# Kernel tuning notes

Hardware: AMD Instinct MI355X
Metric: run time of the kernel (lower is better)

Reference implementation:

```python
import jax, jax.numpy as jnp
import numpy as np

B, S, H = 2, 2048, 1024
NH, NKV, HD = 16, 16, 64
R, KF = 16, 4
THETA = 1000000.0


def setup_inputs() -> dict:
    key = jax.random.key(0)
    ks = jax.random.split(key, 16)
    sc = 0.02
    signs = jax.random.randint(ks[13], (1, 1, 1, KF, HD // 2), 0, 2).astype(jnp.float32) * 2 - 1
    cdma = jnp.concatenate([signs, signs], axis=-1)  # [1,1,1,KF,HD]
    return {
        "hidden_states": jax.random.normal(ks[0], (B, S, H), jnp.float32),
        "position_ids": jnp.broadcast_to(jnp.arange(S, dtype=jnp.int32), (B, S)),
        "q_w": jax.random.normal(ks[1], (H, H), jnp.float32) * sc,
        "q_b": jax.random.normal(ks[2], (H,), jnp.float32) * sc,
        "k_w": jax.random.normal(ks[3], (H, H), jnp.float32) * sc,
        "k_b": jax.random.normal(ks[4], (H,), jnp.float32) * sc,
        "v_w": jax.random.normal(ks[5], (H, H), jnp.float32) * sc,
        "v_b": jax.random.normal(ks[6], (H,), jnp.float32) * sc,
        "o_w": jax.random.normal(ks[7], (H, H), jnp.float32) * sc,
        "lora_qA": jax.random.normal(ks[8], (R, H), jnp.float32) * sc,
        "lora_qB": jax.random.normal(ks[9], (H, R), jnp.float32) * sc,
        "lora_vA": jax.random.normal(ks[10], (R, H), jnp.float32) * sc,
        "lora_vB": jax.random.normal(ks[11], (H, R), jnp.float32) * sc,
        "cdma_keys": cdma,
    }


def _rope(q, k, position_ids):
    # cos/sin per HF rotary embedding, theta=1e6 (Qwen1.5)
    inv_freq = 1.0 / (THETA ** (jnp.arange(0, HD, 2, dtype=jnp.float32) / HD))  # [HD/2]
    freqs = position_ids.astype(jnp.float32)[..., None] * inv_freq  # [B,S,HD/2]
    emb = jnp.concatenate([freqs, freqs], axis=-1)  # [B,S,HD]
    cos = jnp.cos(emb)[:, None]  # [B,1,S,HD]
    sin = jnp.sin(emb)[:, None]

    def rot_half(x):
        return jnp.concatenate([-x[..., HD // 2:], x[..., :HD // 2]], axis=-1)

    return q * cos + rot_half(q) * sin, k * cos + rot_half(k) * sin


def reference(hidden_states, position_ids, q_w, q_b, k_w, k_b, v_w, v_b, o_w,
              lora_qA, lora_qB, lora_vA, lora_vB, cdma_keys):
    bsz, q_len, _ = hidden_states.shape
    # base projections + LoRA adjustments (k has no LoRA)
    q = hidden_states @ q_w.T + q_b + (hidden_states @ lora_qA.T) @ lora_qB.T
    k = hidden_states @ k_w.T + k_b
    v = hidden_states @ v_w.T + v_b + (hidden_states @ lora_vA.T) @ lora_vB.T

    q = q.reshape(bsz, q_len, NH, HD).transpose(0, 2, 1, 3)   # [B,NH,S,HD]
    k = k.reshape(bsz, q_len, NKV, HD).transpose(0, 2, 1, 3)  # [B,NKV,S,HD]
    v = v.reshape(bsz, q_len, NKV, HD).transpose(0, 2, 1, 3)

    q, k = _rope(q, k, position_ids)

    # holographic block sign-bind/sum transform (q_len divisible by KF -> no pad)
    n_slots = q_len // KF
    k_blocks = k.reshape(bsz, NKV, n_slots, KF, HD)
    v_blocks = v.reshape(bsz, NKV, n_slots, KF, HD)
    S_K = jnp.sum(k_blocks * cdma_keys, axis=3, keepdims=True)  # [B,NKV,slots,1,HD]
    S_V = jnp.sum(v_blocks * cdma_keys, axis=3, keepdims=True)
    K_noisy = (S_K * cdma_keys).reshape(bsz, NKV, q_len, HD)
    V_noisy = (S_V * cdma_keys).reshape(bsz, NKV, q_len, HD)

    scale = 1.0 / (np.sqrt(HD) * np.sqrt(KF))
    scores = jnp.einsum('bhqd,bhkd->bhqk', q, K_noisy) * scale
    causal = jnp.tril(jnp.ones((q_len, q_len), dtype=bool))
    scores = jnp.where(causal, scores, jnp.float32(-1e9))
    attn = jax.nn.softmax(scores, axis=-1)
    out = jnp.einsum('bhqk,bhkd->bhqd', attn, V_noisy)
    out = out.transpose(0, 2, 1, 3).reshape(bsz, q_len, NH * HD)
    return out @ o_w.T
```

## Files before the change

kernel.cpp:

```cpp
#include <hip/hip_runtime.h>
#include <hip/hip_bf16.h>
#include <math.h>


typedef __bf16 bf16;
typedef __attribute__((ext_vector_type(8))) __bf16 bf16x8;
typedef __attribute__((ext_vector_type(4))) float f32x4;

#define NB 2
#define SEQ 2048
#define HID 1024
#define NHD 16
#define HDD 64

__device__ __forceinline__ void gld_lds16(const void* g, void* l) {
  __builtin_amdgcn_global_load_lds(
      (const __attribute__((address_space(1))) void*)g,
      (__attribute__((address_space(3))) void*)l, 16, 0, 0);
}

__device__ __forceinline__ unsigned pack2bf(float a, float b) {
  unsigned short ua = __builtin_bit_cast(unsigned short, (bf16)a);
  unsigned short ub = __builtin_bit_cast(unsigned short, (bf16)b);
  return ((unsigned)ub << 16) | ua;
}

__global__ __launch_bounds__(256) void prep_wqkv(
    const float* __restrict__ qw, const float* __restrict__ kw,
    const float* __restrict__ vw, const float* __restrict__ qA,
    const float* __restrict__ qB, const float* __restrict__ vA,
    const float* __restrict__ vB, bf16* __restrict__ W) {
  int idx = blockIdx.x * 256 + threadIdx.x;
  if (idx >= 3072 * 1024) return;
  int n = idx >> 10, k = idx & 1023;
  float v;
  if (n < 1024) {
    v = qw[n * 1024 + k];
#pragma unroll
    for (int r = 0; r < 16; ++r) v += qB[n * 16 + r] * qA[r * 1024 + k];
  } else if (n < 2048) {
    v = kw[(n - 1024) * 1024 + k];
  } else {
    int nn = n - 2048;
    v = vw[nn * 1024 + k];
#pragma unroll
    for (int r = 0; r < 16; ++r) v += vB[nn * 16 + r] * vA[r * 1024 + k];
  }
  int seg = k >> 6, cl = k & 63;
  int ch = (cl >> 3) ^ (n & 7);
  W[(size_t)n * 1024 + (seg << 6) + (ch << 3) + (cl & 7)] = (bf16)v;
}

__global__ __launch_bounds__(256) void cvt_swz(const float* __restrict__ src,
                                               bf16* __restrict__ dst,
                                               int total, int cols) {
  int idx = blockIdx.x * 256 + threadIdx.x;
  if (idx >= total) return;
  int r = idx / cols, c = idx - r * cols;
  int seg = c >> 6, cl = c & 63;
  int ch = (cl >> 3) ^ (r & 7);
  dst[(size_t)r * cols + (seg << 6) + (ch << 3) + (cl & 7)] = (bf16)src[idx];
}

__global__ void bias_cat(const float* __restrict__ qb, const float* __restrict__ kb,
                         const float* __restrict__ vb, float* __restrict__ out) {
  int i = blockIdx.x * 256 + threadIdx.x;
  if (i >= 3072) return;
  out[i] = (i < 1024) ? qb[i] : (i < 2048 ? kb[i - 1024] : vb[i - 2048]);
}

__global__ void rope_tab(float* __restrict__ ct, float* __restrict__ st) {
  int idx = blockIdx.x * 256 + threadIdx.x;
  if (idx >= SEQ * 32) return;
  int s = idx >> 5, i = idx & 31;
  double inv = pow(1.0e6, -(double)i / 32.0);
  double a = (double)s * inv;
  ct[idx] = (float)cos(a);
  st[idx] = (float)sin(a);
}

__global__ __launch_bounds__(256) void gemm_bt(
    const bf16* __restrict__ A, const bf16* __restrict__ Bw,
    const float* __restrict__ bias, bf16* __restrict__ Cb,
    float* __restrict__ Cf, int M, int N, int K) {
  __shared__ __align__(16) bf16 As[128 * 64];
  __shared__ __align__(16) bf16 Bs[128 * 64];
  const int tid = threadIdx.x;
  const int lane = tid & 63, w = tid >> 6;
  const int wm = w >> 1, wn = w & 1;
  const int l15 = lane & 15, l4 = lane >> 4;
  const int m0 = blockIdx.y * 128, n0 = blockIdx.x * 128;
  const size_t rowb = (size_t)K * 2;
  const char* gA = (const char*)A + (size_t)m0 * rowb;
  const char* gB = (const char*)Bw + (size_t)n0 * rowb;
  f32x4 acc[4][4] = {};

  for (int k0 = 0; k0 < K; k0 += 64) {
    const char* gAk = gA + k0 * 2;
    const char* gBk = gB + k0 * 2;
#pragma unroll
    for (int i = 0; i < 4; ++i) {
      int idx = i * 256 + tid;
      int row = idx >> 3, ch = idx & 7;
      gld_lds16(gAk + (size_t)row * rowb + ch * 16,
                (char*)As + (i * 256 + (w << 6)) * 16);
      gld_lds16(gBk + (size_t)row * rowb + ch * 16,
                (char*)Bs + (i * 256 + (w << 6)) * 16);
    }
    __syncthreads();
#pragma unroll
    for (int c = 0; c < 2; ++c) {
      bf16x8 af[4], bfr[4];
#pragma unroll
      for (int mi = 0; mi < 4; ++mi) {
        int row = wm * 64 + mi * 16 + l15;
        int ch = (c * 4 + l4) ^ (row & 7);
        af[mi] = *(const bf16x8*)(As + row * 64 + ch * 8);
      }
#pragma unroll
      for (int ni = 0; ni < 4; ++ni) {
        int row = wn * 64 + ni * 16 + l15;
        int ch = (c * 4 + l4) ^ (row & 7);
        bfr[ni] = *(const bf16x8*)(Bs + row * 64 + ch * 8);
      }
#pragma unroll
      for (int mi = 0; mi < 4; ++mi)
#pragma unroll
        for (int ni = 0; ni < 4; ++ni)
          acc[mi][ni] = __builtin_amdgcn_mfma_f32_16x16x32_bf16(
              af[mi], bfr[ni], acc[mi][ni], 0, 0, 0);
    }
    __syncthreads();
  }
#pragma unroll
  for (int mi = 0; mi < 4; ++mi) {
    int rbase = m0 + wm * 64 + mi * 16 + l4 * 4;
#pragma unroll
    for (int ni = 0; ni < 4; ++ni) {
      int col = n0 + wn * 64 + ni * 16 + l15;
      float badd = bias ? bias[col] : 0.0f;
#pragma unroll
      for (int r = 0; r < 4; ++r) {
        float v = acc[mi][ni][r] + badd;
        if (Cf) Cf[(size_t)(rbase + r) * N + col] = v;
        else    Cb[(size_t)(rbase + r) * N + col] = (bf16)v;
      }
    }
  }
}

__global__ __launch_bounds__(256) void rope_q(
    const bf16* __restrict__ qkv, const int* __restrict__ pos,
    const float* __restrict__ ct, const float* __restrict__ st,
    bf16* __restrict__ Qr) {
  int idx = blockIdx.x * 256 + threadIdx.x;
  if (idx >= NB * NHD * SEQ * 32) return;
  int i = idx & 31, h = (idx >> 5) & 15, s = (idx >> 9) & 2047, b = idx >> 20;
  int p = pos[b * SEQ + s];
  float co = ct[p * 32 + i], sn = st[p * 32 + i];
  size_t base = ((size_t)(b * SEQ + s)) * 3072 + h * 64 + i;
  float x = (float)qkv[base], y = (float)qkv[base + 32];
  size_t ob = ((size_t)((b * 16 + h) * SEQ + s)) * 64 + i;
  Qr[ob]      = (bf16)(x * co - y * sn);
  Qr[ob + 32] = (bf16)(y * co + x * sn);
}

__global__ __launch_bounds__(256) void holo_kv(
    const bf16* __restrict__ qkv, const int* __restrict__ pos,
    const float* __restrict__ ct, const float* __restrict__ st,
    const float* __restrict__ cdma, bf16* __restrict__ Kn,
    bf16* __restrict__ Vt) {
  int idx = blockIdx.x * 256 + threadIdx.x;
  if (idx >= NB * NHD * (SEQ / 4) * 32) return;
  int i = idx & 31, slot = (idx >> 5) & 511, h = (idx >> 14) & 15, b = idx >> 18;
  float c[4];
  float SK = 0.f, SK2 = 0.f, SV = 0.f, SV2 = 0.f;
#pragma unroll
  for (int f = 0; f < 4; ++f) {
    int s = slot * 4 + f;
    float cf = cdma[f * 64 + i];
    c[f] = cf;
    size_t base = ((size_t)(b * SEQ + s)) * 3072 + h * 64 + i;
    float kx = (float)qkv[base + 1024], ky = (float)qkv[base + 1024 + 32];
    int p = pos[b * SEQ + s];
    float co = ct[p * 32 + i], sn = st[p * 32 + i];
    SK  += (kx * co - ky * sn) * cf;
    SK2 += (ky * co + kx * sn) * cf;
    SV  += (float)qkv[base + 2048] * cf;
    SV2 += (float)qkv[base + 2048 + 32] * cf;
  }
  size_t hb = (size_t)(b * 16 + h);
#pragma unroll
  for (int f = 0; f < 4; ++f) {
    int s = slot * 4 + f;
    size_t krow = (hb * SEQ + s) * 64;
    int ch0 = (i >> 3) ^ (s & 7);
    int ch1 = (4 + (i >> 3)) ^ (s & 7);
    Kn[krow + ch0 * 8 + (i & 7)] = (bf16)(SK * c[f]);
    Kn[krow + ch1 * 8 + (i & 7)] = (bf16)(SK2 * c[f]);
    int seg = s >> 6, cl = s & 63;
    int vch = (cl >> 3) ^ (i & 7);
    size_t vrow0 = (hb * 64 + i) * (size_t)SEQ + (seg << 6);
    size_t vrow1 = (hb * 64 + i + 32) * (size_t)SEQ + (seg << 6);
    Vt[vrow0 + vch * 8 + (cl & 7)] = (bf16)(SV * c[f]);
    Vt[vrow1 + vch * 8 + (cl & 7)] = (bf16)(SV2 * c[f]);
  }
}

__global__ __launch_bounds__(256) void attn_fwd(
    const bf16* __restrict__ Qr, const bf16* __restrict__ Kn,
    const bf16* __restrict__ Vt, bf16* __restrict__ AO) {
  __shared__ __align__(16) bf16 Kt[2][64 * 64];
  __shared__ __align__(16) bf16 Vl[2][64 * 64];
  __shared__ __align__(16) bf16 Pt[4][16 * 64];
  const int pq = blockIdx.x, h = blockIdx.y, b = blockIdx.z;
  const int tid = threadIdx.x, lane = tid & 63, w = tid >> 6;
  const int l15 = lane & 15, l4 = lane >> 4;
  const size_t hd = ((size_t)(b * 16 + h)) * SEQ * 64;
  const char* gK0 = (const char*)(Kn + hd);
  const char* gV0 = (const char*)(Vt + hd);
  char* pw = (char*)&Pt[w][0];
  const float sc = (1.0f / 16.0f) * 1.44269504f;

#pragma unroll 1
  for (int phase = 0; phase < 2; ++phase) {
    const int qt = phase ? (31 - pq) : pq;
    const int q0 = qt * 64;
    const int qg = q0 + w * 16 + l15;
    const int nt = qt + 1;

    const bf16* qb = Qr + hd + (size_t)(q0 + w * 16 + l15) * 64;
    bf16x8 qf0 = *(const bf16x8*)(qb + l4 * 8);
    bf16x8 qf1 = *(const bf16x8*)(qb + 32 + l4 * 8);

    f32x4 oacc[4] = {};
    float m = -1e30f, lsum = 0.0f;

#pragma unroll
    for (int i = 0; i < 2; ++i) {
      int idx = i * 256 + tid;
      int row = idx >> 3, ch = idx & 7;
      gld_lds16(gK0 + (size_t)row * 128 + ch * 16,
                (char*)Kt[0] + (i * 256 + (w << 6)) * 16);
      gld_lds16(gV0 + (size_t)row * (SEQ * 2) + ch * 16,
                (char*)Vl[0] + (i * 256 + (w << 6)) * 16);
    }

#pragma unroll 1
    for (int t = 0; t < nt; ++t) {
      const int cur = t & 1;
      if (t + 1 < nt) {
        const int tn = t + 1, s = cur ^ 1;
#pragma unroll
        for (int i = 0; i < 2; ++i) {
          int idx = i * 256 + tid;
          int row = idx >> 3, ch = idx & 7;
          gld_lds16(gK0 + (size_t)(tn * 64 + row) * 128 + ch * 16,
                    (char*)Kt[s] + (i * 256 + (w << 6)) * 16);
          gld_lds16(gV0 + (size_t)row * (SEQ * 2) + tn * 128 + ch * 16,
                    (char*)Vl[s] + (i * 256 + (w << 6)) * 16);
        }
        asm volatile("s_waitcnt vmcnt(4)\ns_barrier" ::: "memory");
      } else {
        asm volatile("s_waitcnt vmcnt(0)\ns_barrier" ::: "memory");
      }

      const bf16* Ktc = Kt[cur];
      const bf16* Vlc = Vl[cur];
      const int kv0 = t * 64;
      const bool diag = (t == qt);

      f32x4 sacc[4] = {};
#pragma unroll
      for (int c = 0; c < 2; ++c) {
        bf16x8 qf = c ? qf1 : qf0;
#pragma unroll
        for (int nf = 0; nf < 4; ++nf) {
          int row = nf * 16 + l15;
          int ch = (c * 4 + l4) ^ (row & 7);
          bf16x8 kf = *(const bf16x8*)(Ktc + row * 64 + ch * 8);
          sacc[nf] = __builtin_amdgcn_mfma_f32_16x16x32_bf16(kf, qf, sacc[nf], 0, 0, 0);
        }
      }

      float pmax = -1e30f;
#pragma unroll
      for (int nf = 0; nf < 4; ++nf)
#pragma unroll
        for (int r = 0; r < 4; ++r) {
          float v = sacc[nf][r] * sc;
          if (diag) {
            int kvg = kv0 + nf * 16 + l4 * 4 + r;
            if (kvg > qg) v = -1e30f;
          }
          sacc[nf][r] = v;
          pmax = fmaxf(pmax, v);
        }
      pmax = fmaxf(pmax, __shfl_xor(pmax, 16));
      pmax = fmaxf(pmax, __shfl_xor(pmax, 32));

      float mn = fmaxf(m, pmax);
      float al = exp2f(m - mn);
      m = mn;
      float rs = 0.0f;
#pragma unroll
      for (int nf = 0; nf < 4; ++nf)
#pragma unroll
        for (int r = 0; r < 4; ++r) {
          float e = exp2f(sacc[nf][r] - m);
          sacc[nf][r] = e;
          rs += e;
        }
      rs += __shfl_xor(rs, 16);
      rs += __shfl_xor(rs, 32);
      lsum = lsum * al + rs;

      float alo[4];
#pragma unroll
      for (int r = 0; r < 4; ++r) alo[r] = __shfl(al, l4 * 4 + r, 64);
#pragma unroll
      for (int df = 0; df < 4; ++df) {
        f32x4 o = oacc[df];
        o[0] *= alo[0]; o[1] *= alo[1]; o[2] *= alo[2]; o[3] *= alo[3];
        oacc[df] = o;
      }

#pragma unroll
      for (int nf = 0; nf < 4; ++nf)
#pragma unroll
        for (int rp = 0; rp < 2; ++rp) {
          unsigned u = pack2bf(sacc[nf][rp * 2], sacc[nf][rp * 2 + 1]);
          int boff = l15 * 128 + (nf * 16 + l4 * 4 + rp * 2) * 2;
          boff ^= (l15 & 7) << 4;
          *(unsigned*)(pw + boff) = u;
        }

#pragma unroll
      for (int c = 0; c < 2; ++c) {
        int pb = (l15 * 128 + c * 64 + l4 * 16) ^ ((l15 & 7) << 4);
        bf16x8 pf = *(const bf16x8*)(pw + pb);
#pragma unroll
        for (int df = 0; df < 4; ++df) {
          int vrow = df * 16 + l15;
          int vch = (c * 4 + l4) ^ (vrow & 7);
          bf16x8 vf = *(const bf16x8*)(Vlc + vrow * 64 + vch * 8);
          oacc[df] = __builtin_amdgcn_mfma_f32_16x16x32_bf16(pf, vf, oacc[df], 0, 0, 0);
        }
      }
      asm volatile("s_barrier" ::: "memory");
    }

    float linv[4];
#pragma unroll
    for (int r = 0; r < 4; ++r) linv[r] = 1.0f / __shfl(lsum, l4 * 4 + r, 64);
#pragma unroll
    for (int df = 0; df < 4; ++df)
#pragma unroll
      for (int r = 0; r < 4; ++r) {
        int s = q0 + w * 16 + l4 * 4 + r;
        int cl = df * 16 + l15;
        int ch = (cl >> 3) ^ (s & 7);
        AO[((size_t)(b * SEQ + s)) * HID + h * 64 + ch * 8 + (cl & 7)] =
            (bf16)(oacc[df][r] * linv[r]);
      }
  }
}

extern "C" void kernel_launch(void* const* d_in, const int* in_sizes, int n_in,
                              void* d_out, int out_size, void* d_ws, size_t ws_size,
                              hipStream_t stream) {
  const float* hs  = (const float*)d_in[0];
  const int* pos   = (const int*)d_in[1];
  const float* qw  = (const float*)d_in[2];
  const float* qb_ = (const float*)d_in[3];
  const float* kw  = (const float*)d_in[4];
  const float* kb_ = (const float*)d_in[5];
  const float* vw  = (const float*)d_in[6];
  const float* vb_ = (const float*)d_in[7];
  const float* ow  = (const float*)d_in[8];
  const float* qA  = (const float*)d_in[9];
  const float* qB  = (const float*)d_in[10];
  const float* vA  = (const float*)d_in[11];
  const float* vB  = (const float*)d_in[12];
  const float* cd  = (const float*)d_in[13];

  char* p = (char*)d_ws;
  auto alloc = [&](size_t bytes) {
    char* r = p; p += (bytes + 255) & ~(size_t)255; return r;
  };
  bf16* hsb   = (bf16*)alloc((size_t)4096 * 1024 * 2);
  bf16* Wqkv  = (bf16*)alloc((size_t)3072 * 1024 * 2);
  float* bqkv = (float*)alloc(3072 * 4);
  bf16* owb   = (bf16*)alloc((size_t)1024 * 1024 * 2);
  bf16* qkvb  = (bf16*)alloc((size_t)4096 * 3072 * 2);
  float* ct   = (float*)alloc((size_t)SEQ * 32 * 4);
  float* st   = (float*)alloc((size_t)SEQ * 32 * 4);
  bf16* Qrb   = (bf16*)alloc((size_t)NB * NHD * SEQ * 64 * 2);
  bf16* Knb   = (bf16*)alloc((size_t)NB * NHD * SEQ * 64 * 2);
  bf16* Vtb   = (bf16*)alloc((size_t)NB * NHD * 64 * SEQ * 2);
  bf16* AOb   = (bf16*)alloc((size_t)4096 * 1024 * 2);

  prep_wqkv<<<dim3(3072 * 1024 / 256), 256, 0, stream>>>(qw, kw, vw, qA, qB, vA, vB, Wqkv);
  cvt_swz<<<dim3(4096 * 1024 / 256), 256, 0, stream>>>(hs, hsb, 4096 * 1024, 1024);
  cvt_swz<<<dim3(1024 * 1024 / 256), 256, 0, stream>>>(ow, owb, 1024 * 1024, 1024);
  bias_cat<<<dim3(12), 256, 0, stream>>>(qb_, kb_, vb_, bqkv);
  rope_tab<<<dim3(SEQ * 32 / 256), 256, 0, stream>>>(ct, st);
  gemm_bt<<<dim3(3072 / 128, 4096 / 128), 256, 0, stream>>>(
      hsb, Wqkv, bqkv, qkvb, nullptr, 4096, 3072, 1024);
  rope_q<<<dim3(NB * NHD * SEQ * 32 / 256), 256, 0, stream>>>(qkvb, pos, ct, st, Qrb);
  holo_kv<<<dim3(NB * NHD * (SEQ / 4) * 32 / 256), 256, 0, stream>>>(
      qkvb, pos, ct, st, cd, Knb, Vtb);
  attn_fwd<<<dim3(16, NHD, NB), 256, 0, stream>>>(Qrb, Knb, Vtb, AOb);
  gemm_bt<<<dim3(1024 / 128, 4096 / 128), 256, 0, stream>>>(
      AOb, owb, nullptr, nullptr, (float*)d_out, 4096, 1024, 1024);
}
```

Measured before the change: 177.3 us.

## Give each attention block one query tile and skip unneeded softmax rescales

Replaces the paired-tile scheme, where each block processed tile pq and tile 31-pq, with one query tile per block and a grid doubled to 32 tiles, launched largest-first. The PV MFMA operands are swapped so each lane owns one query row, which removes the per-row shuffles for the rescale factor and the final normalizer. The rescale of the accumulator and running sum is now skipped when no row's max increased. s_setprio is raised around the MFMA sections. Per-block work is uneven again, and scheduling relies on reverse launch order to balance the load.

```diff
diff --git a/kernel.cpp b/kernel.cpp
--- a/kernel.cpp
+++ b/kernel.cpp
@@ -213,157 +213,149 @@
   __shared__ __align__(16) bf16 Kt[2][64 * 64];
   __shared__ __align__(16) bf16 Vl[2][64 * 64];
   __shared__ __align__(16) bf16 Pt[4][16 * 64];
-  const int pq = blockIdx.x, h = blockIdx.y, b = blockIdx.z;
+  const int qt = 31 - blockIdx.x, h = blockIdx.y, b = blockIdx.z;
   const int tid = threadIdx.x, lane = tid & 63, w = tid >> 6;
   const int l15 = lane & 15, l4 = lane >> 4;
+  const int q0 = qt * 64;
+  const int qg = q0 + w * 16 + l15;
+  const int nt = qt + 1;
   const size_t hd = ((size_t)(b * 16 + h)) * SEQ * 64;
   const char* gK0 = (const char*)(Kn + hd);
   const char* gV0 = (const char*)(Vt + hd);
   char* pw = (char*)&Pt[w][0];
   const float sc = (1.0f / 16.0f) * 1.44269504f;
 
+  const bf16* qb = Qr + hd + (size_t)qg * 64;
+  bf16x8 qf0 = *(const bf16x8*)(qb + l4 * 8);
+  bf16x8 qf1 = *(const bf16x8*)(qb + 32 + l4 * 8);
+
+  f32x4 oacc[4] = {};
+  float m = -1e30f, lsum = 0.0f;
+
+#pragma unroll
+  for (int i = 0; i < 2; ++i) {
+    int idx = i * 256 + tid;
+    int row = idx >> 3, ch = idx & 7;
+    gld_lds16(gK0 + (size_t)row * 128 + ch * 16,
+              (char*)Kt[0] + (i * 256 + (w << 6)) * 16);
+    gld_lds16(gV0 + (size_t)row * (SEQ * 2) + ch * 16,
+              (char*)Vl[0] + (i * 256 + (w << 6)) * 16);
+  }
+
 #pragma unroll 1
-  for (int phase = 0; phase < 2; ++phase) {
-    const int qt = phase ? (31 - pq) : pq;
-    const int q0 = qt * 64;
-    const int qg = q0 + w * 16 + l15;
-    const int nt = qt + 1;
-
-    const bf16* qb = Qr + hd + (size_t)(q0 + w * 16 + l15) * 64;
-    bf16x8 qf0 = *(const bf16x8*)(qb + l4 * 8);
-    bf16x8 qf1 = *(const bf16x8*)(qb + 32 + l4 * 8);
-
-    f32x4 oacc[4] = {};
-    float m = -1e30f, lsum = 0.0f;
-
-#pragma unroll
-    for (int i = 0; i < 2; ++i) {
-      int idx = i * 256 + tid;
-      int row = idx >> 3, ch = idx & 7;
-      gld_lds16(gK0 + (size_t)row * 128 + ch * 16,
-                (char*)Kt[0] + (i * 256 + (w << 6)) * 16);
-      gld_lds16(gV0 + (size_t)row * (SEQ * 2) + ch * 16,
-                (char*)Vl[0] + (i * 256 + (w << 6)) * 16);
-    }
-
-#pragma unroll 1
-    for (int t = 0; t < nt; ++t) {
-      const int cur = t & 1;
-      if (t + 1 < nt) {
-        const int tn = t + 1, s = cur ^ 1;
-#pragma unroll
-        for (int i = 0; i < 2; ++i) {
-          int idx = i * 256 + tid;
-          int row = idx >> 3, ch = idx & 7;
-          gld_lds16(gK0 + (size_t)(tn * 64 + row) * 128 + ch * 16,
-                    (char*)Kt[s] + (i * 256 + (w << 6)) * 16);
-          gld_lds16(gV0 + (size_t)row * (SEQ * 2) + tn * 128 + ch * 16,
-                    (char*)Vl[s] + (i * 256 + (w << 6)) * 16);
+  for (int t = 0; t < nt; ++t) {
+    const int cur = t & 1;
+    if (t + 1 < nt) {
+      const int tn = t + 1, s = cur ^ 1;
+#pragma unroll
+      for (int i = 0; i < 2; ++i) {
+        int idx = i * 256 + tid;
+        int row = idx >> 3, ch = idx & 7;
+        gld_lds16(gK0 + (size_t)(tn * 64 + row) * 128 + ch * 16,
+                  (char*)Kt[s] + (i * 256 + (w << 6)) * 16);
+        gld_lds16(gV0 + (size_t)row * (SEQ * 2) + tn * 128 + ch * 16,
+                  (char*)Vl[s] + (i * 256 + (w << 6)) * 16);
+      }
+      asm volatile("s_waitcnt vmcnt(4)\ns_barrier" ::: "memory");
+    } else {
+      asm volatile("s_waitcnt vmcnt(0)\ns_barrier" ::: "memory");
+    }
+
+    const bf16* Ktc = Kt[cur];
+    const bf16* Vlc = Vl[cur];
+    const int kv0 = t * 64;
+    const bool diag = (t == qt);
+
+    f32x4 sacc[4] = {};
+    __builtin_amdgcn_s_setprio(1);
+#pragma unroll
+    for (int c = 0; c < 2; ++c) {
+      bf16x8 qf = c ? qf1 : qf0;
+#pragma unroll
+      for (int nf = 0; nf < 4; ++nf) {
+        int row = nf * 16 + l15;
+        int ch = (c * 4 + l4) ^ (row & 7);
+        bf16x8 kf = *(const bf16x8*)(Ktc + row * 64 + ch * 8);
+        sacc[nf] = __builtin_amdgcn_mfma_f32_16x16x32_bf16(kf, qf, sacc[nf], 0, 0, 0);
+      }
+    }
+    __builtin_amdgcn_s_setprio(0);
+
+    float pmax = -1e30f;
+#pragma unroll
+    for (int nf = 0; nf < 4; ++nf)
+#pragma unroll
+      for (int r = 0; r < 4; ++r) {
+        float v = sacc[nf][r] * sc;
+        if (diag) {
+          int kvg = kv0 + nf * 16 + l4 * 4 + r;
+          if (kvg > qg) v = -1e30f;
         }
-        asm volatile("s_waitcnt vmcnt(4)\ns_barrier" ::: "memory");
-      } else {
-        asm volatile("s_waitcnt vmcnt(0)\ns_barrier" ::: "memory");
-      }
-
-      const bf16* Ktc = Kt[cur];
-      const bf16* Vlc = Vl[cur];
-      const int kv0 = t * 64;
-      const bool diag = (t == qt);
-
-      f32x4 sacc[4] = {};
-#pragma unroll
-      for (int c = 0; c < 2; ++c) {
-        bf16x8 qf = c ? qf1 : qf0;
-#pragma unroll
-        for (int nf = 0; nf < 4; ++nf) {
-          int row = nf * 16 + l15;
-          int ch = (c * 4 + l4) ^ (row & 7);
-          bf16x8 kf = *(const bf16x8*)(Ktc + row * 64 + ch * 8);
-          sacc[nf] = __builtin_amdgcn_mfma_f32_16x16x32_bf16(kf, qf, sacc[nf], 0, 0, 0);
-        }
-      }
-
-      float pmax = -1e30f;
-#pragma unroll
-      for (int nf = 0; nf < 4; ++nf)
-#pragma unroll
-        for (int r = 0; r < 4; ++r) {
-          float v = sacc[nf][r] * sc;
-          if (diag) {
-            int kvg = kv0 + nf * 16 + l4 * 4 + r;
-            if (kvg > qg) v = -1e30f;
-          }
-          sacc[nf][r] = v;
-          pmax = fmaxf(pmax, v);
-        }
-      pmax = fmaxf(pmax, __shfl_xor(pmax, 16));
-      pmax = fmaxf(pmax, __shfl_xor(pmax, 32));
-
+        sacc[nf][r] = v;
+        pmax = fmaxf(pmax, v);
+      }
+    pmax = fmaxf(pmax, __shfl_xor(pmax, 16));
+    pmax = fmaxf(pmax, __shfl_xor(pmax, 32));
+
+    if (!__all(pmax <= m)) {
       float mn = fmaxf(m, pmax);
       float al = exp2f(m - mn);
       m = mn;
-      float rs = 0.0f;
-#pragma unroll
-      for (int nf = 0; nf < 4; ++nf)
-#pragma unroll
-        for (int r = 0; r < 4; ++r) {
-          float e = exp2f(sacc[nf][r] - m);
-          sacc[nf][r] = e;
-          rs += e;
-        }
-      rs += __shfl_xor(rs, 16);
-      rs += __shfl_xor(rs, 32);
-      lsum = lsum * al + rs;
-
-      float alo[4];
-#pragma unroll
-      for (int r = 0; r < 4; ++r) alo[r] = __shfl(al, l4 * 4 + r, 64);
+      lsum *= al;
+#pragma unroll
+      for (int df = 0; df < 4; ++df) oacc[df] *= al;
+    }
+    float rs = 0.0f;
+#pragma unroll
+    for (int nf = 0; nf < 4; ++nf)
+#pragma unroll
+      for (int r = 0; r < 4; ++r) {
+        float e = exp2f(sacc[nf][r] - m);
+        sacc[nf][r] = e;
+        rs += e;
+      }
+    rs += __shfl_xor(rs, 16);
+    rs += __shfl_xor(rs, 32);
+    lsum += rs;
+
+#pragma unroll
+    for (int nf = 0; nf < 4; ++nf)
+#pragma unroll
+      for (int rp = 0; rp < 2; ++rp) {
+        unsigned u = pack2bf(sacc[nf][rp * 2], sacc[nf][rp * 2 + 1]);
+        int boff = l15 * 128 + (nf * 16 + l4 * 4 + rp * 2) * 2;
+        boff ^= (l15 & 7) << 4;
+        *(unsigned*)(pw + boff) = u;
+      }
+
+    __builtin_amdgcn_s_setprio(1);
+#pragma unroll
+    for (int c = 0; c < 2; ++c) {
+      int pb = (l15 * 128 + c * 64 + l4 * 16) ^ ((l15 & 7) << 4);
+      bf16x8 pf = *(const bf16x8*)(pw + pb);
 #pragma unroll
       for (int df = 0; df < 4; ++df) {
-        f32x4 o = oacc[df];
-        o[0] *= alo[0]; o[1] *= alo[1]; o[2] *= alo[2]; o[3] *= alo[3];
-        oacc[df] = o;
-      }
-
-#pragma unroll
-      for (int nf = 0; nf < 4; ++nf)
-#pragma unroll
-        for (int rp = 0; rp < 2; ++rp) {
-          unsigned u = pack2bf(sacc[nf][rp * 2], sacc[nf][rp * 2 + 1]);
-          int boff = l15 * 128 + (nf * 16 + l4 * 4 + rp * 2) * 2;
-          boff ^= (l15 & 7) << 4;
-          *(unsigned*)(pw + boff) = u;
-        }
-
-#pragma unroll
-      for (int c = 0; c < 2; ++c) {
-        int pb = (l15 * 128 + c * 64 + l4 * 16) ^ ((l15 & 7) << 4);
-        bf16x8 pf = *(const bf16x8*)(pw + pb);
-#pragma unroll
-        for (int df = 0; df < 4; ++df) {
-          int vrow = df * 16 + l15;
-          int vch = (c * 4 + l4) ^ (vrow & 7);
-          bf16x8 vf = *(const bf16x8*)(Vlc + vrow * 64 + vch * 8);
-          oacc[df] = __builtin_amdgcn_mfma_f32_16x16x32_bf16(pf, vf, oacc[df], 0, 0, 0);
-        }
-      }
-      asm volatile("s_barrier" ::: "memory");
-    }
-
-    float linv[4];
-#pragma unroll
-    for (int r = 0; r < 4; ++r) linv[r] = 1.0f / __shfl(lsum, l4 * 4 + r, 64);
-#pragma unroll
-    for (int df = 0; df < 4; ++df)
-#pragma unroll
-      for (int r = 0; r < 4; ++r) {
-        int s = q0 + w * 16 + l4 * 4 + r;
-        int cl = df * 16 + l15;
-        int ch = (cl >> 3) ^ (s & 7);
-        AO[((size_t)(b * SEQ + s)) * HID + h * 64 + ch * 8 + (cl & 7)] =
-            (bf16)(oacc[df][r] * linv[r]);
-      }
-  }
+        int vrow = df * 16 + l15;
+        int vch = (c * 4 + l4) ^ (vrow & 7);
+        bf16x8 vf = *(const bf16x8*)(Vlc + vrow * 64 + vch * 8);
+        oacc[df] = __builtin_amdgcn_mfma_f32_16x16x32_bf16(vf, pf, oacc[df], 0, 0, 0);
+      }
+    }
+    __builtin_amdgcn_s_setprio(0);
+    asm volatile("s_barrier" ::: "memory");
+  }
+
+  const float li = 1.0f / lsum;
+  const size_t arow = ((size_t)(b * SEQ + qg)) * HID + h * 64;
+  const int qk7 = qg & 7;
+#pragma unroll
+  for (int df = 0; df < 4; ++df)
+#pragma unroll
+    for (int r = 0; r < 4; ++r) {
+      int d = df * 16 + l4 * 4 + r;
+      int ch = (d >> 3) ^ qk7;
+      AO[arow + ch * 8 + (d & 7)] = (bf16)(oacc[df][r] * li);
+    }
 }
 
 extern "C" void kernel_launch(void* const* d_in, const int* in_sizes, int n_in,
@@ -410,7 +402,7 @@
   rope_q<<<dim3(NB * NHD * SEQ * 32 / 256), 256, 0, stream>>>(qkvb, pos, ct, st, Qrb);
   holo_kv<<<dim3(NB * NHD * (SEQ / 4) * 32 / 256), 256, 0, stream>>>(
       qkvb, pos, ct, st, cd, Knb, Vtb);
-  attn_fwd<<<dim3(16, NHD, NB), 256, 0, stream>>>(Qrb, Knb, Vtb, AOb);
+  attn_fwd<<<dim3(32, NHD, NB), 256, 0, stream>>>(Qrb, Knb, Vtb, AOb);
   gemm_bt<<<dim3(1024 / 128, 4096 / 128), 256, 0, stream>>>(
       AOb, owb, nullptr, nullptr, (float*)d_out, 4096, 1024, 1024);
 }
```

Result: slower. 202.6 us (+14.3%).
